# Optimization experiments

Measured on AMD Instinct MI355X. Metric: run time of the kernel, lower is better.

The kernel has to match this reference:

```python
import jax, jax.numpy as jnp
import numpy as np

N_NODES = 100000
IN_CH = 128
HID = 64
N_EDGES = 1600000
NEG_SLOPE = 0.2


def setup_inputs() -> dict:
    key = jax.random.key(0)
    k1, k2, k3, k4, k5, k6 = jax.random.split(key, 6)
    x = jax.random.normal(k1, (N_NODES, IN_CH), dtype=jnp.float32)
    edge_index = jax.random.randint(k2, (2, N_EDGES), 0, N_NODES, dtype=jnp.int64)
    # Glorot-style init for GATConv params (heads=1)
    s_w = (2.0 / (IN_CH + HID)) ** 0.5
    W = jax.random.normal(k3, (IN_CH, HID), dtype=jnp.float32) * s_w
    s_a = (2.0 / (1 + HID)) ** 0.5
    att_src = jax.random.normal(k4, (HID,), dtype=jnp.float32) * s_a
    att_dst = jax.random.normal(k5, (HID,), dtype=jnp.float32) * s_a
    bias = jnp.zeros((HID,), dtype=jnp.float32)
    return {"x": x, "edge_index": edge_index, "W": W, "att_src": att_src,
            "att_dst": att_dst, "bias": bias}


def reference(x, edge_index, W, att_src, att_dst, bias):
    N = x.shape[0]
    # PyG GATConv default: add self-loops
    loop = jnp.arange(N, dtype=edge_index.dtype)
    src = jnp.concatenate([edge_index[0], loop])  # message source j
    dst = jnp.concatenate([edge_index[1], loop])  # message target i

    h = x @ W                      # [N, HID]
    a_src = h @ att_src            # [N]
    a_dst = h @ att_dst            # [N]

    # per-edge attention logit: LeakyReLU(a_src[j] + a_dst[i])
    e = jax.nn.leaky_relu(a_src[src] + a_dst[dst], NEG_SLOPE)  # [E+N]
    # numerically-stable segment softmax over destination node
    m = jax.ops.segment_max(e, dst, num_segments=N)
    e = jnp.exp(e - m[dst])
    denom = jax.ops.segment_sum(e, dst, num_segments=N)
    alpha = e / (denom[dst] + 1e-16)               # [E+N]

    # scatter-aggregate weighted source features, then bias
    out = jax.ops.segment_sum(alpha[:, None] * h[src], dst, num_segments=N)
    out = out + bias               # [N, HID]
    return out, alpha[:, None]     # alpha shaped [E+N, heads=1]
```

## Files before the change

kernel.cpp:

```cpp
#include <hip/hip_runtime.h>

#define NN 100000
#define IC 128
#define HD 64
#define NEG 0.2f
#define NPB 32
#define NBKT (NN / NPB)
#define CAP 768
#define TILE 8192
#define NIT 8

typedef float f32x4 __attribute__((ext_vector_type(4)));
typedef short s16x8 __attribute__((ext_vector_type(8)));

__device__ __forceinline__ unsigned short f32_to_bf16u(float f) {
  union { float f; unsigned int i; } v;
  v.f = f;
  unsigned int b = v.i;
  b += 0x7FFFu + ((b >> 16) & 1u);
  return (unsigned short)(b >> 16);
}

__global__ __launch_bounds__(256) void k_gemm(const float* __restrict__ x,
                                              const float* __restrict__ W,
                                              const float* __restrict__ att_s,
                                              const float* __restrict__ att_d,
                                              unsigned short* __restrict__ hb,
                                              float* __restrict__ as_,
                                              float* __restrict__ ad_,
                                              int* __restrict__ bktcur) {
  __shared__ unsigned short xb[64 * 128];
  __shared__ unsigned short wt[64 * 128];
  const int tid = threadIdx.x;
  const int n0 = blockIdx.x * 64;
  if (tid < 2 && 2 * blockIdx.x + tid < NBKT) bktcur[2 * blockIdx.x + tid] = 0;

  #pragma unroll
  for (int i = 0; i < 8; ++i) {
    int f = i * 256 + tid;
    int r = f >> 5, k0 = (f & 31) << 2;
    float4 v = make_float4(0.f, 0.f, 0.f, 0.f);
    if (n0 + r < NN) v = *(const float4*)&x[(size_t)(n0 + r) * IC + k0];
    ushort4 u;
    u.x = f32_to_bf16u(v.x); u.y = f32_to_bf16u(v.y);
    u.z = f32_to_bf16u(v.z); u.w = f32_to_bf16u(v.w);
    int idx = r * 128 + k0;
    *(ushort4*)&xb[idx ^ ((r & 7) << 3)] = u;
  }
  #pragma unroll
  for (int i = 0; i < 8; ++i) {
    int f = i * 256 + tid;
    int k = f >> 4, c0 = (f & 15) << 2;
    float4 v = *(const float4*)&W[k * HD + c0];
    const float* vf = (const float*)&v;
    #pragma unroll
    for (int j = 0; j < 4; ++j) {
      int c = c0 + j;
      int idx = c * 128 + k;
      wt[idx ^ ((c & 7) << 3)] = f32_to_bf16u(vf[j]);
    }
  }
  __syncthreads();

  const int wv = tid >> 6, lane = tid & 63;
  const int fr = lane & 15;
  const int fq = lane >> 4;
  const int nodeR = wv * 16 + fr;
  f32x4 acc[4] = {};
  #pragma unroll
  for (int kb = 0; kb < 4; ++kb) {
    int ks = kb * 32 + fq * 8;
    int ia = nodeR * 128 + ks;
    s16x8 af = *(s16x8*)&xb[ia ^ ((nodeR & 7) << 3)];
    #pragma unroll
    for (int cg = 0; cg < 4; ++cg) {
      int col = cg * 16 + fr;
      int ib = col * 128 + ks;
      s16x8 bfr = *(s16x8*)&wt[ib ^ ((col & 7) << 3)];
      acc[cg] = __builtin_amdgcn_mfma_f32_16x16x32_bf16(af, bfr, acc[cg], 0, 0, 0);
    }
  }

  float atts[4], attd[4];
  #pragma unroll
  for (int cg = 0; cg < 4; ++cg) {
    atts[cg] = att_s[cg * 16 + fr];
    attd[cg] = att_d[cg * 16 + fr];
  }
  __syncthreads();
  unsigned short* ho = xb;

  #pragma unroll
  for (int j = 0; j < 4; ++j) {
    int nrel = wv * 16 + fq * 4 + j;
    float ps = acc[0][j]*atts[0] + acc[1][j]*atts[1]
             + acc[2][j]*atts[2] + acc[3][j]*atts[3];
    float pd = acc[0][j]*attd[0] + acc[1][j]*attd[1]
             + acc[2][j]*attd[2] + acc[3][j]*attd[3];
    #pragma unroll
    for (int mk = 1; mk < 16; mk <<= 1) {
      ps += __shfl_xor(ps, mk);
      pd += __shfl_xor(pd, mk);
    }
    if (fr == 0 && n0 + nrel < NN) { as_[n0 + nrel] = ps; ad_[n0 + nrel] = pd; }
    #pragma unroll
    for (int cg = 0; cg < 4; ++cg)
      ho[nrel * 72 + cg * 16 + fr] = f32_to_bf16u(acc[cg][j]);
  }
  __syncthreads();

  {
    int node = tid >> 2, ch = (tid & 3) << 4;
    if (n0 + node < NN) {
      ushort4 a0 = *(ushort4*)&ho[node * 72 + ch];
      ushort4 a1 = *(ushort4*)&ho[node * 72 + ch + 4];
      ushort4 a2 = *(ushort4*)&ho[node * 72 + ch + 8];
      ushort4 a3 = *(ushort4*)&ho[node * 72 + ch + 12];
      unsigned short* dst = &hb[(size_t)(n0 + node) * HD + ch];
      *(ushort4*)(dst) = a0;
      *(ushort4*)(dst + 4) = a1;
      *(ushort4*)(dst + 8) = a2;
      *(ushort4*)(dst + 12) = a3;
    }
  }
}

__global__ __launch_bounds__(1024) void k_part(const int* __restrict__ ei,
                                               const float* __restrict__ as_,
                                               const float* __restrict__ ad_,
                                               int* __restrict__ bktcur,
                                               int2* __restrict__ bktbuf,
                                               float* __restrict__ p_lin,
                                               int E, int M) {
  __shared__ int lcnt[NBKT];
  __shared__ int gbs[NBKT];
  const int tid = threadIdx.x;
  const int base = blockIdx.x * TILE;

  for (int c = tid; c < NBKT; c += 1024) lcnt[c] = 0;
  __syncthreads();

  int pkx[NIT], rb[NIT];
  float tv[NIT];
  #pragma unroll
  for (int i = 0; i < NIT; ++i) {
    int m = base + i * 1024 + tid;
    if (m < M) {
      int s, d;
      if (m < E) { s = ei[m]; d = ei[E + m]; }
      else       { s = m - E; d = s; }
      int b = d >> 5;
      pkx[i] = (s << 5) | (d & 31);
      tv[i] = as_[s] + ad_[d];
      int r = atomicAdd(&lcnt[b], 1);
      rb[i] = (b << 13) | r;
    } else rb[i] = -1;
  }
  __syncthreads();

  for (int c = tid; c < NBKT; c += 1024) {
    int v = lcnt[c];
    gbs[c] = v ? atomicAdd(&bktcur[c], v) : 0;
  }
  __syncthreads();

  #pragma unroll
  for (int i = 0; i < NIT; ++i) {
    if (rb[i] >= 0) {
      int m = base + i * 1024 + tid;
      float t = tv[i];
      t = t > 0.f ? t : NEG * t;
      float p = __expf(t);
      p_lin[m] = p;
      int b = (unsigned)rb[i] >> 13, r = rb[i] & 8191;
      int slot = gbs[b] + r;
      if (slot < CAP)
        bktbuf[(size_t)b * CAP + slot] = make_int2(pkx[i], __float_as_int(p));
    }
  }
}

__global__ __launch_bounds__(256) void k_pg(const int* __restrict__ bktcur,
                                            const int2* __restrict__ bktbuf,
                                            const unsigned short* __restrict__ hb,
                                            const float* __restrict__ bias,
                                            float* __restrict__ out,
                                            float* __restrict__ denom) {
  __shared__ int2 sp[CAP];
  __shared__ int cnt2[NPB], nstart[NPB], cur[NPB];
  __shared__ float dls[NPB];
  const int b = blockIdx.x;
  const int d0 = b << 5;
  const int tid = threadIdx.x;
  const int cnt = min(bktcur[b], CAP);
  const int2* mybuf = bktbuf + (size_t)b * CAP;
  const char* hbb = (const char*)hb;

  if (tid < NPB) cnt2[tid] = 0;
  __syncthreads();
  for (int e = tid; e < cnt; e += 256) atomicAdd(&cnt2[mybuf[e].x & 31], 1);
  __syncthreads();

  if (tid < 32) {
    int a = cnt2[tid];
    int va = a;
    #pragma unroll
    for (int off = 1; off < 32; off <<= 1) {
      int na = __shfl_up(va, off);
      if (tid >= off) va += na;
    }
    nstart[tid] = va - a;
    cur[tid] = va - a;
  }
  __syncthreads();
  for (int e = tid; e < cnt; e += 256) {
    int2 v = mybuf[e];
    int slot = atomicAdd(&cur[v.x & 31], 1);
    sp[slot] = make_int2((v.x & ~31) << 2, v.y);
  }
  __syncthreads();

  const int wv = tid >> 6, lane = tid & 63;
  const int half = lane >> 5;
  const int hl = lane & 31;
  const unsigned chb = (unsigned)hl << 2;
  const float2 bs2 = *(const float2*)&bias[2 * hl];

  for (int n = wv; n < NPB; n += 4) {
    int beg = nstart[n], end = beg + cnt2[n];
    float ax = 0.f, ay = 0.f, dens = 0.f;
    int e = beg;
    for (; e + 8 <= end; e += 8) {
      #pragma unroll
      for (int j = 0; j < 4; ++j) {
        int2 v = sp[e + 2 * j + half];
        unsigned u = *(const unsigned*)(hbb + ((unsigned)v.x + chb));
        float p = __int_as_float(v.y);
        dens += p;
        ax += p * __uint_as_float(u << 16);
        ay += p * __uint_as_float(u & 0xffff0000u);
      }
    }
    {
      #pragma unroll
      for (int j = 0; j < 4; ++j) {
        int idx = e + 2 * j + half;
        if (idx < end) {
          int2 v = sp[idx];
          unsigned u = *(const unsigned*)(hbb + ((unsigned)v.x + chb));
          float p = __int_as_float(v.y);
          dens += p;
          ax += p * __uint_as_float(u << 16);
          ay += p * __uint_as_float(u & 0xffff0000u);
        }
      }
    }
    ax += __shfl_xor(ax, 32);
    ay += __shfl_xor(ay, 32);
    dens += __shfl_xor(dens, 32);
    if (half == 0) {
      float rd = 1.f / (dens + 1e-16f);
      float2 o;
      o.x = ax * rd + bs2.x;
      o.y = ay * rd + bs2.y;
      *(float2*)&out[(size_t)(d0 + n) * HD + 2 * hl] = o;
      if (hl == 0) dls[n] = dens;
    }
  }
  __syncthreads();
  if (tid < NPB) denom[d0 + tid] = dls[tid];
}

__global__ __launch_bounds__(256) void k_alpha(const int* __restrict__ ei,
                                               const float* __restrict__ p_lin,
                                               const float* __restrict__ denom,
                                               float* __restrict__ alpha_out,
                                               int E, int M) {
  int m = blockIdx.x * 256 + threadIdx.x;
  if (m >= M) return;
  int d = (m < E) ? ei[E + m] : (m - E);
  alpha_out[m] = p_lin[m] / (denom[d] + 1e-16f);
}

extern "C" void kernel_launch(void* const* d_in, const int* in_sizes, int n_in,
                              void* d_out, int out_size, void* d_ws, size_t ws_size,
                              hipStream_t stream) {
  const float* x     = (const float*)d_in[0];
  const int*   ei    = (const int*)d_in[1];
  const float* W     = (const float*)d_in[2];
  const float* att_s = (const float*)d_in[3];
  const float* att_d = (const float*)d_in[4];
  const float* bias  = (const float*)d_in[5];

  const int E = in_sizes[1] / 2;
  const int M = E + NN;

  float* out       = (float*)d_out;
  float* alpha_out = out + (size_t)NN * HD;

  char* w = (char*)d_ws;
  auto alloc = [&](size_t bytes) {
    char* p = w;
    w += (bytes + 15) & ~(size_t)15;
    return p;
  };
  unsigned short* hb = (unsigned short*)alloc(sizeof(unsigned short) * (size_t)NN * HD);
  float* as_    = (float*)alloc(sizeof(float) * NN);
  float* ad_    = (float*)alloc(sizeof(float) * NN);
  float* denom  = (float*)alloc(sizeof(float) * NN);
  float* p_lin  = (float*)alloc(sizeof(float) * (size_t)M);
  int*   bktcur = (int*)alloc(sizeof(int) * NBKT);
  int2*  bktbuf = (int2*)alloc(sizeof(int2) * (size_t)NBKT * CAP);

  k_gemm<<<(NN + 63) / 64, 256, 0, stream>>>(x, W, att_s, att_d, hb, as_, ad_,
                                             bktcur);
  k_part<<<(M + TILE - 1) / TILE, 1024, 0, stream>>>(ei, as_, ad_, bktcur,
                                                     bktbuf, p_lin, E, M);
  k_pg<<<NBKT, 256, 0, stream>>>(bktcur, bktbuf, hb, bias, out, denom);
  k_alpha<<<(M + 255) / 256, 256, 0, stream>>>(ei, p_lin, denom, alpha_out,
                                               E, M);
}
```

Baseline: 111.4 us.

## Replace global-atomic bucket buffers with per-tile local sort and offset table

The partition kernel no longer reserves slots in global per-bucket buffers through global atomics. Each 8192-edge tile now does a local counting sort by bucket, using a block-wide prefix scan in shared memory, and writes its sorted tile plus a per-tile bucket offset row. The gather kernel then walks every tile's offset row to collect its bucket's edges. This removes the global atomics and the bktcur reset in the GEMM. In exchange, each gather block reads about 208 offset rows with short, scattered, serial per-thread loops, which may cost more than the atomics it replaces.

```diff
diff --git a/kernel.cpp b/kernel.cpp
--- a/kernel.cpp
+++ b/kernel.cpp
@@ -8,7 +8,8 @@
 #define NBKT (NN / NPB)
 #define CAP 768
 #define TILE 8192
-#define NIT 8
+#define NIT 16
+#define LSTRIDE (NBKT + 11)
 
 typedef float f32x4 __attribute__((ext_vector_type(4)));
 typedef short s16x8 __attribute__((ext_vector_type(8)));
@@ -27,13 +28,11 @@
                                               const float* __restrict__ att_d,
                                               unsigned short* __restrict__ hb,
                                               float* __restrict__ as_,
-                                              float* __restrict__ ad_,
-                                              int* __restrict__ bktcur) {
+                                              float* __restrict__ ad_) {
   __shared__ unsigned short xb[64 * 128];
   __shared__ unsigned short wt[64 * 128];
   const int tid = threadIdx.x;
   const int n0 = blockIdx.x * 64;
-  if (tid < 2 && 2 * blockIdx.x + tid < NBKT) bktcur[2 * blockIdx.x + tid] = 0;
 
   #pragma unroll
   for (int i = 0; i < 8; ++i) {
@@ -125,26 +124,27 @@
   }
 }
 
-__global__ __launch_bounds__(1024) void k_part(const int* __restrict__ ei,
-                                               const float* __restrict__ as_,
-                                               const float* __restrict__ ad_,
-                                               int* __restrict__ bktcur,
-                                               int2* __restrict__ bktbuf,
-                                               float* __restrict__ p_lin,
-                                               int E, int M) {
+__global__ __launch_bounds__(512) void k_part(const int* __restrict__ ei,
+                                              const float* __restrict__ as_,
+                                              const float* __restrict__ ad_,
+                                              int2* __restrict__ sorted,
+                                              int* __restrict__ lofs,
+                                              float* __restrict__ p_lin,
+                                              int E, int M) {
   __shared__ int lcnt[NBKT];
-  __shared__ int gbs[NBKT];
+  __shared__ int wpart[8];
   const int tid = threadIdx.x;
-  const int base = blockIdx.x * TILE;
-
-  for (int c = tid; c < NBKT; c += 1024) lcnt[c] = 0;
+  const int blk = blockIdx.x;
+  const int base = blk * TILE;
+
+  for (int c = tid; c < NBKT; c += 512) lcnt[c] = 0;
   __syncthreads();
 
   int pkx[NIT], rb[NIT];
   float tv[NIT];
   #pragma unroll
   for (int i = 0; i < NIT; ++i) {
-    int m = base + i * 1024 + tid;
+    int m = base + i * 512 + tid;
     if (m < M) {
       int s, d;
       if (m < E) { s = ei[m]; d = ei[E + m]; }
@@ -158,47 +158,82 @@
   }
   __syncthreads();
 
-  for (int c = tid; c < NBKT; c += 1024) {
-    int v = lcnt[c];
-    gbs[c] = v ? atomicAdd(&bktcur[c], v) : 0;
-  }
-  __syncthreads();
+  {
+    int a[7];
+    int base7 = tid * 7, lsum = 0;
+    #pragma unroll
+    for (int j = 0; j < 7; ++j) {
+      int idx = base7 + j;
+      a[j] = (idx < NBKT) ? lcnt[idx] : 0;
+      lsum += a[j];
+    }
+    int v = lsum;
+    #pragma unroll
+    for (int off = 1; off < 64; off <<= 1) {
+      int nv = __shfl_up(v, off);
+      if ((tid & 63) >= off) v += nv;
+    }
+    if ((tid & 63) == 63) wpart[tid >> 6] = v;
+    __syncthreads();
+    int woff = 0;
+    for (int w0 = 0; w0 < (tid >> 6); ++w0) woff += wpart[w0];
+    int start = woff + v - lsum;
+    #pragma unroll
+    for (int j = 0; j < 7; ++j) {
+      int idx = base7 + j;
+      if (idx < NBKT) { lcnt[idx] = start; start += a[j]; }
+    }
+  }
+  __syncthreads();
+
+  {
+    int* row = lofs + (size_t)blk * LSTRIDE;
+    for (int c = tid; c < NBKT; c += 512) row[c] = lcnt[c];
+    if (tid == 0) {
+      int tot = min(M - base, TILE);
+      row[NBKT] = tot;
+    }
+  }
 
   #pragma unroll
   for (int i = 0; i < NIT; ++i) {
     if (rb[i] >= 0) {
-      int m = base + i * 1024 + tid;
+      int m = base + i * 512 + tid;
       float t = tv[i];
       t = t > 0.f ? t : NEG * t;
       float p = __expf(t);
       p_lin[m] = p;
       int b = (unsigned)rb[i] >> 13, r = rb[i] & 8191;
-      int slot = gbs[b] + r;
-      if (slot < CAP)
-        bktbuf[(size_t)b * CAP + slot] = make_int2(pkx[i], __float_as_int(p));
-    }
-  }
-}
-
-__global__ __launch_bounds__(256) void k_pg(const int* __restrict__ bktcur,
-                                            const int2* __restrict__ bktbuf,
+      sorted[(size_t)blk * TILE + lcnt[b] + r] =
+          make_int2(pkx[i], __float_as_int(p));
+    }
+  }
+}
+
+__global__ __launch_bounds__(256) void k_pg(const int* __restrict__ lofs,
+                                            const int2* __restrict__ sorted,
                                             const unsigned short* __restrict__ hb,
                                             const float* __restrict__ bias,
                                             float* __restrict__ out,
-                                            float* __restrict__ denom) {
+                                            float* __restrict__ denom,
+                                            int npart) {
   __shared__ int2 sp[CAP];
   __shared__ int cnt2[NPB], nstart[NPB], cur[NPB];
   __shared__ float dls[NPB];
   const int b = blockIdx.x;
   const int d0 = b << 5;
   const int tid = threadIdx.x;
-  const int cnt = min(bktcur[b], CAP);
-  const int2* mybuf = bktbuf + (size_t)b * CAP;
   const char* hbb = (const char*)hb;
 
   if (tid < NPB) cnt2[tid] = 0;
   __syncthreads();
-  for (int e = tid; e < cnt; e += 256) atomicAdd(&cnt2[mybuf[e].x & 31], 1);
+
+  for (int t = tid; t < npart; t += 256) {
+    const int* row = lofs + (size_t)t * LSTRIDE;
+    int st = row[b], en = row[b + 1];
+    const int2* src = sorted + (size_t)t * TILE;
+    for (int e = st; e < en; ++e) atomicAdd(&cnt2[src[e].x & 31], 1);
+  }
   __syncthreads();
 
   if (tid < 32) {
@@ -213,10 +248,16 @@
     cur[tid] = va - a;
   }
   __syncthreads();
-  for (int e = tid; e < cnt; e += 256) {
-    int2 v = mybuf[e];
-    int slot = atomicAdd(&cur[v.x & 31], 1);
-    sp[slot] = make_int2((v.x & ~31) << 2, v.y);
+
+  for (int t = tid; t < npart; t += 256) {
+    const int* row = lofs + (size_t)t * LSTRIDE;
+    int st = row[b], en = row[b + 1];
+    const int2* src = sorted + (size_t)t * TILE;
+    for (int e = st; e < en; ++e) {
+      int2 v = src[e];
+      int slot = atomicAdd(&cur[v.x & 31], 1);
+      if (slot < CAP) sp[slot] = make_int2((v.x & ~31) << 2, v.y);
+    }
   }
   __syncthreads();
 
@@ -227,7 +268,7 @@
   const float2 bs2 = *(const float2*)&bias[2 * hl];
 
   for (int n = wv; n < NPB; n += 4) {
-    int beg = nstart[n], end = beg + cnt2[n];
+    int beg = nstart[n], end = min(beg + cnt2[n], CAP);
     float ax = 0.f, ay = 0.f, dens = 0.f;
     int e = beg;
     for (; e + 8 <= end; e += 8) {
@@ -294,6 +335,7 @@
 
   const int E = in_sizes[1] / 2;
   const int M = E + NN;
+  const int npart = (M + TILE - 1) / TILE;
 
   float* out       = (float*)d_out;
   float* alpha_out = out + (size_t)NN * HD;
@@ -309,14 +351,12 @@
   float* ad_    = (float*)alloc(sizeof(float) * NN);
   float* denom  = (float*)alloc(sizeof(float) * NN);
   float* p_lin  = (float*)alloc(sizeof(float) * (size_t)M);
-  int*   bktcur = (int*)alloc(sizeof(int) * NBKT);
-  int2*  bktbuf = (int2*)alloc(sizeof(int2) * (size_t)NBKT * CAP);
-
-  k_gemm<<<(NN + 63) / 64, 256, 0, stream>>>(x, W, att_s, att_d, hb, as_, ad_,
-                                             bktcur);
-  k_part<<<(M + TILE - 1) / TILE, 1024, 0, stream>>>(ei, as_, ad_, bktcur,
-                                                     bktbuf, p_lin, E, M);
-  k_pg<<<NBKT, 256, 0, stream>>>(bktcur, bktbuf, hb, bias, out, denom);
+  int*   lofs   = (int*)alloc(sizeof(int) * (size_t)npart * LSTRIDE);
+  int2*  sorted = (int2*)alloc(sizeof(int2) * (size_t)npart * TILE);
+
+  k_gemm<<<(NN + 63) / 64, 256, 0, stream>>>(x, W, att_s, att_d, hb, as_, ad_);
+  k_part<<<npart, 512, 0, stream>>>(ei, as_, ad_, sorted, lofs, p_lin, E, M);
+  k_pg<<<NBKT, 256, 0, stream>>>(lofs, sorted, hb, bias, out, denom, npart);
   k_alpha<<<(M + 255) / 256, 256, 0, stream>>>(ei, p_lin, denom, alpha_out,
                                                E, M);
 }
```

After: 152.2 us. +36.6%, slower.
